# Optimization experiments

Hardware: AMD Instinct MI355X
Metric: run time of the kernel (lower is better)

Reference implementation:

```python
import jax, jax.numpy as jnp
import numpy as np

N_HEAD = 12
N_EMBED = 768

def setup_inputs() -> dict:
    key = jax.random.key(0)
    ks = jax.random.split(key, 5)
    B, T, C = 8, 1024, N_EMBED
    s_in = 1.0 / np.sqrt(C)
    s3 = 1.0 / np.sqrt(3 * C)
    return {
        "x": jax.random.normal(ks[0], (B, T, C), dtype=jnp.float32),
        "W_qkv": jax.random.normal(ks[1], (C, 3 * C), dtype=jnp.float32) * s_in,
        "b_qkv": jnp.zeros((3 * C,), dtype=jnp.float32),
        "W_out": jax.random.normal(ks[2], (C, C), dtype=jnp.float32) * s_in,
        "b_out": jnp.zeros((C,), dtype=jnp.float32),
    }

def reference(x, W_qkv, b_qkv, W_out, b_out):
    B, T, C = x.shape
    H = N_HEAD
    d_k = C // H
    qkv = x @ W_qkv + b_qkv  # [B,T,3C]
    q, k, v = jnp.split(qkv, 3, axis=-1)
    # [B,H,T,d]
    q = q.reshape(B, T, H, d_k).transpose(0, 2, 1, 3)
    k = k.reshape(B, T, H, d_k).transpose(0, 2, 1, 3)
    v = v.reshape(B, T, H, d_k).transpose(0, 2, 1, 3)
    logits = jnp.einsum('bhqd,bhkd->bhqk', q, k) * (d_k ** -0.5)
    causal = jnp.tril(jnp.ones((T, T), dtype=bool))
    logits = jnp.where(causal, logits, -jnp.inf)
    scores = jax.nn.softmax(logits, axis=-1)
    out = jnp.einsum('bhqk,bhkd->bhqd', scores, v)
    out = out.transpose(0, 2, 1, 3).reshape(B, T, C)
    return out @ W_out + b_out
```

## Files before the change

kernel.cpp:

```cpp
#include <hip/hip_runtime.h>
#include <stdint.h>

#define B_ 8
#define T_ 1024
#define C_ 768
#define H_ 12
#define DK 64
#define BT (B_*T_)
#define NQKV (3*C_)

typedef unsigned short u16;
typedef __bf16 bf16x8 __attribute__((ext_vector_type(8)));
typedef __bf16 bf16x4 __attribute__((ext_vector_type(4)));
typedef float  f32x4  __attribute__((ext_vector_type(4)));

typedef const __attribute__((address_space(1))) void gvoid_t;
typedef __attribute__((address_space(3))) void lvoid_t;

#define SBARRIER()  asm volatile("s_barrier" ::: "memory")
#define SWAITCNT(s) asm volatile("s_waitcnt " s ::: "memory")

__device__ __forceinline__ void gl_lds16(const void* g, void* l) {
    __builtin_amdgcn_global_load_lds((gvoid_t*)g, (lvoid_t*)l, 16, 0, 0);
}

__device__ __forceinline__ u16 f2b(float f) {
    union { float f; unsigned int u; } v; v.f = f;
    unsigned int u = v.u;
    return (u16)((u + 0x7fffu + ((u >> 16) & 1u)) >> 16);
}

__device__ __forceinline__ f32x4 mfma16(bf16x8 a, bf16x8 b, f32x4 c) {
    return __builtin_amdgcn_mfma_f32_16x16x32_bf16(a, b, c, 0, 0, 0);
}

__global__ __launch_bounds__(256)
void k_prep(const float* __restrict__ x, u16* __restrict__ xb,
            const float* __restrict__ wqkv, u16* __restrict__ wqkvT,
            const float* __restrict__ wout, u16* __restrict__ woutT)
{
    __shared__ u16 tile[32][34];
    const int bid = blockIdx.x;
    const int tid = threadIdx.x;
    if (bid < 6144) {
        int i = bid * 256 + tid;
        float4 f = ((const float4*)x)[i];
        uint2 o;
        o.x = (unsigned)f2b(f.x) | ((unsigned)f2b(f.y) << 16);
        o.y = (unsigned)f2b(f.z) | ((unsigned)f2b(f.w) << 16);
        ((uint2*)xb)[i] = o;
        return;
    }
    const float* w; u16* wt; int K, N, n0, k0;
    if (bid < 6144 + 1728) {
        int idx = bid - 6144;
        w = wqkv; wt = wqkvT; K = C_; N = NQKV;
        n0 = (idx % 72) * 32; k0 = (idx / 72) * 32;
    } else {
        int idx = bid - 7872;
        w = wout; wt = woutT; K = C_; N = C_;
        n0 = (idx % 24) * 32; k0 = (idx / 24) * 32;
    }
    const int tx = tid & 31, ty = tid >> 5;
    #pragma unroll
    for (int i = 0; i < 4; i++)
        tile[ty + i * 8][tx] = f2b(w[(size_t)(k0 + ty + i * 8) * N + n0 + tx]);
    __syncthreads();
    #pragma unroll
    for (int i = 0; i < 4; i++)
        wt[(size_t)(n0 + ty + i * 8) * K + k0 + tx] = tile[tx][ty + i * 8];
}

__global__ __launch_bounds__(256, 2)
void k_gemm_qkv(const u16* __restrict__ A, const u16* __restrict__ Bt,
                const float* __restrict__ bias,
                u16* __restrict__ qo, u16* __restrict__ ko, u16* __restrict__ vto)
{
    const int K = C_;
    __shared__ u16 As[3][128 * 32];
    __shared__ u16 Bs[3][288 * 32];
    const int tid  = threadIdx.x;
    const int lane = tid & 63;
    const int w    = tid >> 6;
    const int quad = lane >> 4;
    const int col  = lane & 15;

    const int id   = blockIdx.x + gridDim.x * blockIdx.y;
    const int xcd  = id & 7;
    const int slot = id >> 3;
    const int m0   = (xcd * 8 + (slot & 7)) * 128;
    const int n0   = (slot >> 3) * 96;

    const int wm   = w * 32;

    f32x4 zero4 = {0.f, 0.f, 0.f, 0.f};
    f32x4 acc[2][18];
    #pragma unroll
    for (int i = 0; i < 2; i++)
        #pragma unroll
        for (int j = 0; j < 18; j++) acc[i][j] = zero4;

    const int sr  = tid >> 2;
    const int scc = ((tid & 3) ^ ((sr >> 1) & 3)) * 8;
    const u16* gA = A  + (size_t)(m0 + sr) * K + scc;
    const u16* gB = Bt + (size_t)(n0 + sr) * K + scc;

    const int NIT = K >> 5;

    #define STAGE(kt, bufi)                                                               \
        do {                                                                              \
            gl_lds16(gA + (kt),                  (char*)As[bufi] + w * 1024);             \
            gl_lds16(gA + (size_t)64 * K + (kt), (char*)As[bufi] + 4096 + w * 1024);      \
            _Pragma("unroll")                                                             \
            for (int s = 0; s < 3; s++) {                                                 \
                const u16* gBs = gB + (size_t)(s * C_) * K;                               \
                gl_lds16(gBs + (kt), (char*)Bs[bufi] + s * 6144 + w * 1024);              \
                if (w < 2)                                                                \
                    gl_lds16(gBs + (size_t)64 * K + (kt),                                 \
                             (char*)Bs[bufi] + s * 6144 + 4096 + w * 1024);               \
            }                                                                             \
        } while (0)

    STAGE(0, 0);
    STAGE(32, 1);
    int cur = 0;
    for (int it = 0; it < NIT; ++it) {
        if (it + 1 < NIT) {
            if (w < 2) { SWAITCNT("vmcnt(8)"); } else { SWAITCNT("vmcnt(5)"); }
        } else {
            SWAITCNT("vmcnt(0)");
        }
        SBARRIER();
        if (it + 2 < NIT) {
            int b2 = cur + 2; if (b2 >= 3) b2 -= 3;
            STAGE((it + 2) << 5, b2);
        }

        const u16* Ab = As[cur];
        const u16* Bb = Bs[cur];
        bf16x8 af[2];
        #pragma unroll
        for (int mt = 0; mt < 2; mt++) {
            int row = wm + mt * 16 + col;
            af[mt] = *(const bf16x8*)&Ab[row * 32 + ((quad ^ ((row >> 1) & 3)) * 8)];
        }
        #pragma unroll
        for (int nt = 0; nt < 18; nt++) {
            int row = nt * 16 + col;
            bf16x8 bfr = *(const bf16x8*)&Bb[row * 32 + ((quad ^ ((row >> 1) & 3)) * 8)];
            acc[0][nt] = mfma16(af[0], bfr, acc[0][nt]);
            acc[1][nt] = mfma16(af[1], bfr, acc[1][nt]);
        }

        cur = (cur == 2) ? 0 : cur + 1;
    }
    #undef STAGE

    #pragma unroll
    for (int mt = 0; mt < 2; mt++) {
        #pragma unroll
        for (int nt = 0; nt < 18; nt++) {
            const int sec = nt / 6;
            const int cc  = n0 + (nt - sec * 6) * 16 + col;
            const int h   = cc >> 6;
            const int d   = cc & 63;
            #pragma unroll
            for (int r = 0; r < 4; r++) {
                int m = m0 + wm + mt * 16 + quad * 4 + r;
                int b = m >> 10;
                int t = m & 1023;
                int bh = b * H_ + h;
                float v = acc[mt][nt][r] + bias[sec * C_ + cc];
                u16 bv = f2b(v);
                if (sec == 0)      qo [((size_t)bh * T_ + t) * DK + d] = bv;
                else if (sec == 1) ko [((size_t)bh * T_ + t) * DK + d] = bv;
                else               vto[((size_t)bh * DK + d) * T_ + t] = bv;
            }
        }
    }
}

__global__ __launch_bounds__(256, 4)
void k_gemm_out(const u16* __restrict__ A, const u16* __restrict__ Bt,
                const float* __restrict__ bias, float* __restrict__ outf)
{
    const int K = C_, N = C_;
    __shared__ u16 As[3][128 * 32];
    __shared__ u16 Bs[3][64 * 32];
    const int tid  = threadIdx.x;
    const int lane = tid & 63;
    const int w    = tid >> 6;
    const int quad = lane >> 4;
    const int col  = lane & 15;

    const int id   = blockIdx.x;
    const int xcd  = id & 7;
    const int slot = id >> 3;
    const int m0   = (xcd * 8 + (slot & 7)) * 128;
    const int n0   = (slot >> 3) * 64;

    f32x4 zero4 = {0.f, 0.f, 0.f, 0.f};
    f32x4 acc[2][4];
    #pragma unroll
    for (int i = 0; i < 2; i++)
        #pragma unroll
        for (int j = 0; j < 4; j++) acc[i][j] = zero4;

    const int sr  = tid >> 2;
    const int scc = ((tid & 3) ^ ((sr >> 1) & 3)) * 8;
    const u16* gA = A  + (size_t)(m0 + sr) * K + scc;
    const u16* gB = Bt + (size_t)(n0 + sr) * K + scc;

    const int NIT = K >> 5;

    #define STAGE(kt, bufi)                                                          \
        do {                                                                         \
            gl_lds16(gA + (kt),                  (char*)As[bufi] + w * 1024);        \
            gl_lds16(gA + (size_t)64 * K + (kt), (char*)As[bufi] + 4096 + w * 1024); \
            gl_lds16(gB + (kt),                  (char*)Bs[bufi] + w * 1024);        \
        } while (0)

    STAGE(0, 0);
    STAGE(32, 1);
    int cur = 0;
    for (int it = 0; it < NIT; ++it) {
        if (it + 1 < NIT) {
            SWAITCNT("vmcnt(3)");
        } else {
            SWAITCNT("vmcnt(0)");
        }
        SBARRIER();
        if (it + 2 < NIT) {
            int b2 = cur + 2; if (b2 >= 3) b2 -= 3;
            STAGE((it + 2) << 5, b2);
        }

        const u16* Ab = As[cur];
        const u16* Bb = Bs[cur];
        bf16x8 af[2], bfr[4];
        #pragma unroll
        for (int mt = 0; mt < 2; mt++) {
            int row = w * 32 + mt * 16 + col;
            af[mt] = *(const bf16x8*)&Ab[row * 32 + ((quad ^ ((row >> 1) & 3)) * 8)];
        }
        #pragma unroll
        for (int nt = 0; nt < 4; nt++) {
            int row = nt * 16 + col;
            bfr[nt] = *(const bf16x8*)&Bb[row * 32 + ((quad ^ ((row >> 1) & 3)) * 8)];
        }
        #pragma unroll
        for (int mt = 0; mt < 2; mt++)
            #pragma unroll
            for (int nt = 0; nt < 4; nt++)
                acc[mt][nt] = mfma16(af[mt], bfr[nt], acc[mt][nt]);

        cur = (cur == 2) ? 0 : cur + 1;
    }
    #undef STAGE

    #pragma unroll
    for (int mt = 0; mt < 2; mt++) {
        #pragma unroll
        for (int nt = 0; nt < 4; nt++) {
            #pragma unroll
            for (int r = 0; r < 4; r++) {
                int m = m0 + w * 32 + mt * 16 + quad * 4 + r;
                int n = n0 + nt * 16 + col;
                outf[(size_t)m * N + n] = acc[mt][nt][r] + bias[n];
            }
        }
    }
}

#define PSTRIDE 72

__device__ __forceinline__ bf16x8 ld_sw(const u16* base, int row, int half,
                                        int quad, int c7) {
    return *(const bf16x8*)(base + row * DK + (((half * 4 + quad) ^ c7) * 8));
}

template <bool MASK>
__device__ __forceinline__ void attn_chunk(
    const u16* Ks, const u16* Vs, __bf16* pbuf,
    const bf16x8 (&qf)[2][2], bf16x8 ones,
    int kv0, int qw, int quad, int col,
    f32x4 (&oacc)[2][4], f32x4 (&lacc)[2])
{
    const int c7 = col & 7;
    f32x4 zero4 = {0.f, 0.f, 0.f, 0.f};
    f32x4 st[2][4];
    #pragma unroll
    for (int g = 0; g < 4; g++) {
        bf16x8 klo = ld_sw(Ks, g * 16 + col, 0, quad, c7);
        bf16x8 khi = ld_sw(Ks, g * 16 + col, 1, quad, c7);
        st[0][g] = mfma16(khi, qf[0][1], mfma16(klo, qf[0][0], zero4));
        st[1][g] = mfma16(khi, qf[1][1], mfma16(klo, qf[1][0], zero4));
    }
    const float scl = 0.18033688f;
    #pragma unroll
    for (int s = 0; s < 2; s++) {
        __bf16* pb = pbuf + s * 16 * PSTRIDE + col * PSTRIDE;
        #pragma unroll
        for (int g = 0; g < 4; g++) {
            bf16x4 pp;
            #pragma unroll
            for (int r = 0; r < 4; r++) {
                float p = __builtin_amdgcn_exp2f(st[s][g][r] * scl - 12.0f);
                if (MASK) {
                    int kv = kv0 + g * 16 + quad * 4 + r;
                    if (kv > qw + s * 16 + col) p = 0.f;
                }
                pp[r] = (__bf16)p;
            }
            *(bf16x4*)(pb + g * 16 + quad * 4) = pp;
        }
    }
    SWAITCNT("lgkmcnt(0)");
    bf16x8 pf[2][2];
    #pragma unroll
    for (int s = 0; s < 2; s++) {
        const __bf16* pb = pbuf + s * 16 * PSTRIDE + col * PSTRIDE;
        pf[s][0] = *(const bf16x8*)(pb + quad * 8);
        pf[s][1] = *(const bf16x8*)(pb + 32 + quad * 8);
        lacc[s] = mfma16(pf[s][1], ones, mfma16(pf[s][0], ones, lacc[s]));
    }
    #pragma unroll
    for (int dt = 0; dt < 4; dt++) {
        bf16x8 vlo = ld_sw(Vs, dt * 16 + col, 0, quad, c7);
        bf16x8 vhi = ld_sw(Vs, dt * 16 + col, 1, quad, c7);
        #pragma unroll
        for (int s = 0; s < 2; s++)
            oacc[s][dt] = mfma16(pf[s][1], vhi, mfma16(pf[s][0], vlo, oacc[s][dt]));
    }
}

__global__ __launch_bounds__(256, 3)
void k_attn(const u16* __restrict__ Q, const u16* __restrict__ Kf,
            const u16* __restrict__ Vt, u16* __restrict__ Of)
{
    __shared__ u16 Ks[2][64 * DK];
    __shared__ u16 Vs[2][64 * DK];
    __shared__ __bf16 Plds[4][32 * PSTRIDE];
    const int bh   = blockIdx.x;
    const int b    = bh / H_;
    const int h    = bh - b * H_;
    const int tid  = threadIdx.x;
    const int lane = tid & 63;
    const int w    = tid >> 6;
    const int quad = lane >> 4;
    const int col  = lane & 15;
    const int ty   = 7 - (int)blockIdx.y;
    const int nch  = 2 * ty + 2;
    const int qw   = ty * 128 + w * 32;
    __bf16* pbuf = Plds[w];

    const u16* Qb = Q  + (size_t)bh * T_ * DK;
    const u16* Kb = Kf + (size_t)bh * T_ * DK;
    const u16* Vb = Vt + (size_t)bh * DK * T_;

    int sG0 = tid, sG1 = 256 + tid;
    int sr0 = sG0 >> 3, sg0 = (sG0 & 7) ^ (sr0 & 7);
    int sr1 = sG1 >> 3, sg1 = (sG1 & 7) ^ (sr1 & 7);

    bf16x8 qf[2][2];
    #pragma unroll
    for (int s = 0; s < 2; s++) {
        const u16* qp = Qb + (size_t)(qw + s * 16 + col) * DK;
        qf[s][0] = *(const bf16x8*)(qp + quad * 8);
        qf[s][1] = *(const bf16x8*)(qp + 32 + quad * 8);
    }

    bf16x8 ones;
    #pragma unroll
    for (int i = 0; i < 8; i++) ((u16*)&ones)[i] = 0x3F80;

    f32x4 zero4 = {0.f, 0.f, 0.f, 0.f};
    f32x4 oacc[2][4];
    f32x4 lacc[2] = {zero4, zero4};
    #pragma unroll
    for (int s = 0; s < 2; s++)
        #pragma unroll
        for (int dt = 0; dt < 4; dt++) oacc[s][dt] = zero4;

    #define ASTAGE(c, bufi)                                                            \
        do {                                                                           \
            int kvs = (c) * 64;                                                        \
            gl_lds16(Kb + (size_t)(kvs + sr0) * DK + sg0 * 8, (char*)Ks[bufi] + w * 1024);        \
            gl_lds16(Kb + (size_t)(kvs + sr1) * DK + sg1 * 8, (char*)Ks[bufi] + 4096 + w * 1024); \
            gl_lds16(Vb + (size_t)sr0 * T_ + kvs + sg0 * 8,   (char*)Vs[bufi] + w * 1024);        \
            gl_lds16(Vb + (size_t)sr1 * T_ + kvs + sg1 * 8,   (char*)Vs[bufi] + 4096 + w * 1024); \
        } while (0)

    ASTAGE(0, 0);
    #pragma unroll 1
    for (int c = 0; c < nch; ++c) {
        const int cur = c & 1;
        SWAITCNT("vmcnt(0)");
        SBARRIER();
        if (c + 1 < nch) {
            ASTAGE(c + 1, cur ^ 1);
        }

        const int kv0 = c * 64;
        if (kv0 <= qw + 31) {
            if (kv0 + 63 <= qw)
                attn_chunk<false>(Ks[cur], Vs[cur], pbuf, qf, ones, kv0, qw, quad, col, oacc, lacc);
            else
                attn_chunk<true>(Ks[cur], Vs[cur], pbuf, qf, ones, kv0, qw, quad, col, oacc, lacc);
        }
    }
    #undef ASTAGE

    #pragma unroll
    for (int s = 0; s < 2; s++) {
        #pragma unroll
        for (int r = 0; r < 4; r++) {
            float inv = 1.f / lacc[s][r];
            int t = qw + s * 16 + quad * 4 + r;
            u16* op = Of + ((size_t)(b * T_ + t)) * C_ + h * DK;
            #pragma unroll
            for (int dt = 0; dt < 4; dt++) op[dt * 16 + col] = f2b(oacc[s][dt][r] * inv);
        }
    }
}

extern "C" void kernel_launch(void* const* d_in, const int* in_sizes, int n_in,
                              void* d_out, int out_size, void* d_ws, size_t ws_size,
                              hipStream_t stream) {
    const float* x    = (const float*)d_in[0];
    const float* Wqkv = (const float*)d_in[1];
    const float* bqkv = (const float*)d_in[2];
    const float* Wout = (const float*)d_in[3];
    const float* bout = (const float*)d_in[4];
    float* out = (float*)d_out;

    char* ws = (char*)d_ws;
    u16* xb    = (u16*)(ws);
    u16* wqkvT = (u16*)(ws + 12582912);
    u16* woutT = (u16*)(ws + 16121856);
    u16* qw    = (u16*)(ws + 17301504);
    u16* kw    = (u16*)(ws + 29884416);
    u16* vtw   = (u16*)(ws + 42467328);
    u16* aw    = (u16*)(ws + 55050240);

    k_prep<<<8448, 256, 0, stream>>>(x, xb, Wqkv, wqkvT, Wout, woutT);

    k_gemm_qkv<<<dim3(8, BT / 128), 256, 0, stream>>>(
        xb, wqkvT, bqkv, qw, kw, vtw);

    k_attn<<<dim3(B_ * H_, 8), 256, 0, stream>>>(qw, kw, vtw, aw);

    k_gemm_out<<<768, 256, 0, stream>>>(aw, woutT, bout, out);
}
```

Baseline: 175.7 us.

## Widen out-projection GEMM tile to 128x96 with double-buffered 64-wide K stages

The output-projection GEMM tile grows from 128x64 to 128x96, so the grid shrinks from 768 to 512 blocks and each A tile is reused across more columns. The K loop moves from a triple-buffered 32-wide pipeline to a double-buffered 64-wide one, with a full vmcnt(0) wait before each barrier. This halves the number of barriers and raises MFMA work per LDS load. In exchange it uses more LDS and registers per block, lowers the occupancy hint to 2, and loses the partial-wait prefetch overlap.

Measured after the change: 172.6 us. Within noise of the previous version (-1.8%).

```diff
diff --git a/kernel.cpp b/kernel.cpp
--- a/kernel.cpp
+++ b/kernel.cpp
@@ -180,13 +180,13 @@
     }
 }
 
-__global__ __launch_bounds__(256, 4)
+__global__ __launch_bounds__(256, 2)
 void k_gemm_out(const u16* __restrict__ A, const u16* __restrict__ Bt,
                 const float* __restrict__ bias, float* __restrict__ outf)
 {
     const int K = C_, N = C_;
-    __shared__ u16 As[3][128 * 32];
-    __shared__ u16 Bs[3][64 * 32];
+    __shared__ u16 As[2][2][128 * 32];
+    __shared__ u16 Bs[2][2][96 * 32];
     const int tid  = threadIdx.x;
     const int lane = tid & 63;
     const int w    = tid >> 6;
@@ -197,74 +197,74 @@
     const int xcd  = id & 7;
     const int slot = id >> 3;
     const int m0   = (xcd * 8 + (slot & 7)) * 128;
-    const int n0   = (slot >> 3) * 64;
+    const int n0   = (slot >> 3) * 96;
+
+    const int wm   = w * 32;
 
     f32x4 zero4 = {0.f, 0.f, 0.f, 0.f};
-    f32x4 acc[2][4];
+    f32x4 acc[2][6];
     #pragma unroll
     for (int i = 0; i < 2; i++)
         #pragma unroll
-        for (int j = 0; j < 4; j++) acc[i][j] = zero4;
+        for (int j = 0; j < 6; j++) acc[i][j] = zero4;
 
     const int sr  = tid >> 2;
     const int scc = ((tid & 3) ^ ((sr >> 1) & 3)) * 8;
     const u16* gA = A  + (size_t)(m0 + sr) * K + scc;
     const u16* gB = Bt + (size_t)(n0 + sr) * K + scc;
 
-    const int NIT = K >> 5;
-
-    #define STAGE(kt, bufi)                                                          \
-        do {                                                                         \
-            gl_lds16(gA + (kt),                  (char*)As[bufi] + w * 1024);        \
-            gl_lds16(gA + (size_t)64 * K + (kt), (char*)As[bufi] + 4096 + w * 1024); \
-            gl_lds16(gB + (kt),                  (char*)Bs[bufi] + w * 1024);        \
+    const int NT64 = K >> 6;
+
+    #define SUB(kt, bufi, subi)                                                           \
+        do {                                                                              \
+            gl_lds16(gA + (kt),                  (char*)As[bufi][subi] + w * 1024);       \
+            gl_lds16(gA + (size_t)64 * K + (kt), (char*)As[bufi][subi] + 4096 + w * 1024);\
+            gl_lds16(gB + (kt),                  (char*)Bs[bufi][subi] + w * 1024);       \
+            if (w < 2)                                                                    \
+                gl_lds16(gB + (size_t)64 * K + (kt), (char*)Bs[bufi][subi] + 4096 + w * 1024);\
         } while (0)
+    #define STAGE(t, bufi)  do { SUB(((t) << 6), bufi, 0); SUB(((t) << 6) + 32, bufi, 1); } while (0)
 
     STAGE(0, 0);
-    STAGE(32, 1);
-    int cur = 0;
-    for (int it = 0; it < NIT; ++it) {
-        if (it + 1 < NIT) {
-            SWAITCNT("vmcnt(3)");
-        } else {
-            SWAITCNT("vmcnt(0)");
-        }
+    for (int it = 0; it < NT64; ++it) {
+        const int cur = it & 1;
+        SWAITCNT("vmcnt(0)");
         SBARRIER();
-        if (it + 2 < NIT) {
-            int b2 = cur + 2; if (b2 >= 3) b2 -= 3;
-            STAGE((it + 2) << 5, b2);
-        }
-
-        const u16* Ab = As[cur];
-        const u16* Bb = Bs[cur];
-        bf16x8 af[2], bfr[4];
-        #pragma unroll
-        for (int mt = 0; mt < 2; mt++) {
-            int row = w * 32 + mt * 16 + col;
-            af[mt] = *(const bf16x8*)&Ab[row * 32 + ((quad ^ ((row >> 1) & 3)) * 8)];
-        }
-        #pragma unroll
-        for (int nt = 0; nt < 4; nt++) {
-            int row = nt * 16 + col;
-            bfr[nt] = *(const bf16x8*)&Bb[row * 32 + ((quad ^ ((row >> 1) & 3)) * 8)];
-        }
-        #pragma unroll
-        for (int mt = 0; mt < 2; mt++)
-            #pragma unroll
-            for (int nt = 0; nt < 4; nt++)
-                acc[mt][nt] = mfma16(af[mt], bfr[nt], acc[mt][nt]);
-
-        cur = (cur == 2) ? 0 : cur + 1;
+        if (it + 1 < NT64)
+            STAGE(it + 1, cur ^ 1);
+
+        #pragma unroll
+        for (int kk = 0; kk < 2; ++kk) {
+            const u16* Ab = As[cur][kk];
+            const u16* Bb = Bs[cur][kk];
+            bf16x8 af[2], bfr[6];
+            #pragma unroll
+            for (int mt = 0; mt < 2; mt++) {
+                int row = wm + mt * 16 + col;
+                af[mt] = *(const bf16x8*)&Ab[row * 32 + ((quad ^ ((row >> 1) & 3)) * 8)];
+            }
+            #pragma unroll
+            for (int nt = 0; nt < 6; nt++) {
+                int row = nt * 16 + col;
+                bfr[nt] = *(const bf16x8*)&Bb[row * 32 + ((quad ^ ((row >> 1) & 3)) * 8)];
+            }
+            #pragma unroll
+            for (int mt = 0; mt < 2; mt++)
+                #pragma unroll
+                for (int nt = 0; nt < 6; nt++)
+                    acc[mt][nt] = mfma16(af[mt], bfr[nt], acc[mt][nt]);
+        }
     }
     #undef STAGE
+    #undef SUB
 
     #pragma unroll
     for (int mt = 0; mt < 2; mt++) {
         #pragma unroll
-        for (int nt = 0; nt < 4; nt++) {
+        for (int nt = 0; nt < 6; nt++) {
             #pragma unroll
             for (int r = 0; r < 4; r++) {
-                int m = m0 + w * 32 + mt * 16 + quad * 4 + r;
+                int m = m0 + wm + mt * 16 + quad * 4 + r;
                 int n = n0 + nt * 16 + col;
                 outf[(size_t)m * N + n] = acc[mt][nt][r] + bias[n];
             }
@@ -450,5 +450,5 @@
 
     k_attn<<<dim3(B_ * H_, 8), 256, 0, stream>>>(qw, kw, vtw, aw);
 
-    k_gemm_out<<<768, 256, 0, stream>>>(aw, woutT, bout, out);
-}
+    k_gemm_out<<<512, 256, 0, stream>>>(aw, woutT, bout, out);
+}
```
